# Kernel optimization log

Measured on AMD Instinct MI355X. Metric: run time of the kernel, lower is better.

The kernel has to match this reference:

```python
import jax, jax.numpy as jnp
import numpy as np

DIM = 128   # dim
KS = 3      # kernel_size
N = 8       # temporal frames (hard-coded n=8 in module)
B = 4       # clip batch -> 2D batch = B*N = 32
H = W = 64
EPS = 1e-5

def _bn(x, g, b, m, v):
    # inference BatchNorm2d over channel axis 1 (NCHW)
    s = g * jax.lax.rsqrt(v + EPS)
    return x * s[None, :, None, None] + (b - m * s)[None, :, None, None]

def _bn_vec(x, g, b, m, v):
    # BatchNorm over last axis of (B, C)
    s = g * jax.lax.rsqrt(v + EPS)
    return x * s + (b - m * s)

def setup_inputs():
    key = jax.random.key(0)
    ks = iter(jax.random.split(key, 48))
    nrm = lambda shape, sc=0.05: jax.random.normal(next(ks), shape, jnp.float32) * sc
    uni = lambda shape: jax.random.uniform(next(ks), shape, jnp.float32, minval=0.5, maxval=1.5)
    def bn_p(c):
        return uni((c,)), nrm((c,)), nrm((c,)), uni((c,))  # gamma, beta, running_mean, running_var
    d = {}
    d["x"] = jax.random.normal(next(ks), (B * N, DIM, H, W), jnp.float32)
    d["w_key"] = nrm((DIM, DIM // 4, KS, 1, 1))                      # conv3d (k,1,1), groups=4, no bias
    d["bnk_g"], d["bnk_b"], d["bnk_m"], d["bnk_v"] = bn_p(DIM)
    d["w_e1"] = nrm((DIM // 2, 2 * DIM))                             # 1x1 conv, no bias
    d["bne_g"], d["bne_b"], d["bne_m"], d["bne_v"] = bn_p(DIM // 2)
    d["w_e2"] = nrm((KS * DIM // 4, DIM // 2))
    d["b_e2"] = nrm((KS * DIM // 4,))
    d["gn_g"] = uni((KS * DIM // 4,))
    d["gn_b"] = nrm((KS * DIM // 4,))
    d["w_1x1"] = nrm((DIM, DIM))                                     # 1x1 conv, no bias
    d["bn1_g"], d["bn1_b"], d["bn1_m"], d["bn1_v"] = bn_p(DIM)
    d["bn2_g"], d["bn2_b"], d["bn2_m"], d["bn2_v"] = bn_p(DIM)
    d["w_se1"] = nrm((DIM, DIM))                                     # attn_chs = max(dim*2//2, 32) = dim
    d["b_se1"] = nrm((DIM,))
    d["bnse_g"], d["bnse_b"], d["bnse_m"], d["bnse_v"] = bn_p(DIM)
    d["w_se2"] = nrm((2 * DIM, DIM))
    d["b_se2"] = nrm((2 * DIM,))
    return d

def reference(x, w_key, bnk_g, bnk_b, bnk_m, bnk_v, w_e1, bne_g, bne_b, bne_m, bne_v,
              w_e2, b_e2, gn_g, gn_b, w_1x1, bn1_g, bn1_b, bn1_m, bn1_v,
              bn2_g, bn2_b, bn2_m, bn2_v, w_se1, b_se1, bnse_g, bnse_b, bnse_m, bnse_v,
              w_se2, b_se2):
    B2, C, Hh, Ww = x.shape
    b = B2 // N
    # --- key_embed: temporal grouped conv3d + BN + ReLU ---
    x5 = x.reshape(b, N, C, Hh, Ww).transpose(0, 2, 1, 3, 4)          # b c n h w
    kk = jax.lax.conv_general_dilated(
        x5, w_key, (1, 1, 1), ((KS // 2, KS // 2), (0, 0), (0, 0)),
        dimension_numbers=('NCDHW', 'OIDHW', 'NCDHW'), feature_group_count=4)
    k2d = kk.transpose(0, 2, 1, 3, 4).reshape(B2, C, Hh, Ww)
    k2d = jax.nn.relu(_bn(k2d, bnk_g, bnk_b, bnk_m, bnk_v))
    # --- dynamic per-pixel temporal kernels ---
    qk = jnp.concatenate([x, k2d], axis=1)                            # (b n) 2c h w
    e = jax.nn.relu(_bn(jnp.einsum('bchw,oc->bohw', qk, w_e1), bne_g, bne_b, bne_m, bne_v))
    wd = jnp.einsum('bchw,oc->bohw', e, w_e2) + b_e2[None, :, None, None]
    # GroupNorm: num_groups = C//4, group size = KS channels -> normalize over (KS, H, W)
    wg = wd.reshape(B2, C // 4, KS, Hh, Ww)
    mu = wg.mean(axis=(2, 3, 4), keepdims=True)
    var = wg.var(axis=(2, 3, 4), keepdims=True)
    wg = (wg - mu) * jax.lax.rsqrt(var + EPS)
    wd = wg.reshape(B2, KS * C // 4, Hh, Ww) * gn_g[None, :, None, None] + gn_b[None, :, None, None]
    wd = wd.reshape(B2, C // 4, KS, Hh, Ww)                           # w.view(b, c//4, 1, k, h, w) with c-dim squeezed
    # --- value path: 1x1 conv + BN, temporal unfold, dynamic aggregation ---
    v = _bn(jnp.einsum('bchw,oc->bohw', x, w_1x1), bn1_g, bn1_b, bn1_m, bn1_v)
    v5 = v.reshape(b, N, C, Hh, Ww).transpose(0, 2, 1, 3, 4)          # b c n h w
    pf = (KS - 1) // 2
    vp = jnp.pad(v5, ((0, 0), (0, 0), (pf, KS - 1 - pf), (0, 0), (0, 0)))
    unf = jnp.stack([vp[:, :, i:i + N] for i in range(KS)], axis=-1)  # b c n h w k (unfold dim=2)
    unf = unf.transpose(0, 2, 1, 3, 4, 5).reshape(B2, C // 4, 4, Hh, Ww, KS)  # (b n) c1 c2 h w k
    agg = jnp.einsum('nckhw,ncdhwk->ncdhw', wd, unf).reshape(B2, C, Hh, Ww)
    agg = _bn(agg, bn2_g, bn2_b, bn2_m, bn2_v)
    agg = agg * jax.nn.sigmoid(agg)                                   # SiLU
    # --- radix-2 split attention over (agg, k) ---
    x6 = agg.reshape(b, N, C, Hh, Ww).transpose(0, 2, 1, 3, 4)        # B C N H W
    k6 = k2d.reshape(b, N, C, Hh, Ww).transpose(0, 2, 1, 3, 4)
    u = jnp.stack([x6, k6], axis=2)                                   # B C 2 N H W
    gap = u.sum(axis=2).mean(axis=(2, 3, 4))                          # B C
    a = jax.nn.relu(_bn_vec(gap @ w_se1.T + b_se1, bnse_g, bnse_b, bnse_m, bnse_v))
    attn = jax.nn.softmax((a @ w_se2.T + b_se2).reshape(b, C, 2), axis=2)
    out = (u * attn[:, :, :, None, None, None]).sum(axis=2)           # B C N H W
    return out.transpose(0, 2, 1, 3, 4).reshape(B2, C, Hh, Ww)
```

## Files before the change

### kernel.cpp

```cpp
#include <hip/hip_runtime.h>

#define EPSV 1e-5f
typedef unsigned short u16;
typedef unsigned int u32;


typedef __attribute__((ext_vector_type(8))) __bf16 bf16x8;
typedef __attribute__((ext_vector_type(4))) float f32x4;
union ABcast { uint4 u; bf16x8 v; };

__device__ __forceinline__ u32 bfbits(float f) {
    u32 u = __float_as_uint(f);
    u += 0x7fff + ((u >> 16) & 1);
    return u >> 16;
}
__device__ __forceinline__ float bflo(u32 p) { return __uint_as_float(p << 16); }
__device__ __forceinline__ float bfhi(u32 p) { return __uint_as_float(p & 0xffff0000u); }

__global__ __launch_bounds__(256) void kW_pack(
    const float* __restrict__ wk, const float* __restrict__ w1,
    const float* __restrict__ we1, const float* __restrict__ we2,
    u32* __restrict__ wkF, u32* __restrict__ wB1,
    u32* __restrict__ wB, u32* __restrict__ wB2)
{
    int i = blockIdx.x * 256 + threadIdx.x;
    if (i < 6144) {
        int jj = i & 3;
        int ln = (i >> 2) & 63;
        int nt = (i >> 8) & 1;
        int rest = i >> 9;
        int grp = rest / 3, dk = rest % 3;
        int n = nt * 16 + (ln & 15);
        int k = (ln >> 4) * 8 + 2 * jj;
        int o = grp * 32 + n;
        wkF[i] = bfbits(wk[o * 96 + k * 3 + dk]) |
                 (bfbits(wk[o * 96 + (k + 1) * 3 + dk]) << 16);
    } else if (i < 14336) {
        int j2 = i - 6144;
        int jj = j2 & 3;
        int ln = (j2 >> 2) & 63;
        int nt = (j2 >> 8) & 7;
        int kb = j2 >> 11;
        int n = nt * 16 + (ln & 15);
        int k = kb * 32 + (ln >> 4) * 8 + 2 * jj;
        wB1[j2] = bfbits(w1[n * 128 + k]) | (bfbits(w1[n * 128 + k + 1]) << 16);
    } else if (i < 22528) {
        int j2 = i - 14336;
        int jj = j2 & 3;
        int ln = (j2 >> 2) & 63;
        int nt = (j2 >> 8) & 3;
        int kb = j2 >> 10;
        int n  = nt * 16 + (ln & 15);
        int k  = kb * 32 + (ln >> 4) * 8 + 2 * jj;
        wB[j2] = bfbits(we1[n * 256 + k]) | (bfbits(we1[n * 256 + k + 1]) << 16);
    } else if (i < 25600) {
        int j2 = i - 22528;
        int jj = j2 & 3;
        int ln = (j2 >> 2) & 63;
        int rest = j2 >> 8;
        int kb = rest / 6, nt = rest % 6;
        int n = nt * 16 + (ln & 15);
        int k = kb * 32 + (ln >> 4) * 8 + 2 * jj;
        wB2[j2] = bfbits(we2[n * 64 + k]) | (bfbits(we2[n * 64 + k + 1]) << 16);
    }
}

__global__ __launch_bounds__(256, 8) void kX_cvt(
    const float* __restrict__ x, u32* __restrict__ xh2)
{
    int qid = blockIdx.x * 256 + threadIdx.x;
    int px  = (qid & 1023) * 4;
    int c2g = qid >> 10;
    const float4 a = *(const float4*)(x + (c2g * 2) * 4096 + px);
    const float4 b = *(const float4*)(x + (c2g * 2 + 1) * 4096 + px);
    uint4 o;
    o.x = bfbits(a.x) | (bfbits(b.x) << 16);
    o.y = bfbits(a.y) | (bfbits(b.y) << 16);
    o.z = bfbits(a.z) | (bfbits(b.z) << 16);
    o.w = bfbits(a.w) | (bfbits(b.w) << 16);
    *(uint4*)(xh2 + c2g * 4096 + px) = o;
}

__global__ __launch_bounds__(256, 4) void kA_key(
    const u32* __restrict__ xh2, const u32* __restrict__ wkF,
    const float* __restrict__ g, const float* __restrict__ bb,
    const float* __restrict__ m, const float* __restrict__ vr,
    u32* __restrict__ k2dh2, float* __restrict__ gap)
{
    int tid  = threadIdx.x;
    int lane = tid & 63;
    int q    = __builtin_amdgcn_readfirstlane(tid >> 6);
    int blk  = blockIdx.x;
    int tile = blk & 15;
    int grp  = (blk >> 4) & 3;
    int b2   = blk >> 6;
    int px0  = tile * 256;
    int bi = b2 >> 3, ni = b2 & 7;
    int lrow = lane & 15, lk = lane >> 4;
    const uint4* wkF4 = (const uint4*)wkF;

    f32x4 acc[4][2];
    #pragma unroll
    for (int mt = 0; mt < 4; ++mt)
        #pragma unroll
        for (int nt = 0; nt < 2; ++nt)
            acc[mt][nt] = (f32x4){0.f, 0.f, 0.f, 0.f};

    int pxA[4];
    #pragma unroll
    for (int mt = 0; mt < 4; ++mt) pxA[mt] = px0 + (4 * q + mt) * 16 + lrow;

    #pragma unroll
    for (int dk = 0; dk < 3; ++dk) {
        int nf = ni + dk - 1;
        if (nf >= 0 && nf < 8) {
            const u32* src = xh2 + ((bi * 8 + nf) * 64 + grp * 16) * 4096;
            int c2b = (lk * 4) * 4096;
            ABcast a[4];
            #pragma unroll
            for (int mt = 0; mt < 4; ++mt) {
                a[mt].u.x = src[c2b         + pxA[mt]];
                a[mt].u.y = src[c2b + 4096  + pxA[mt]];
                a[mt].u.z = src[c2b + 8192  + pxA[mt]];
                a[mt].u.w = src[c2b + 12288 + pxA[mt]];
            }
            #pragma unroll
            for (int nt = 0; nt < 2; ++nt) {
                ABcast bfr;
                bfr.u = wkF4[((grp * 3 + dk) * 2 + nt) * 64 + lane];
                #pragma unroll
                for (int mt = 0; mt < 4; ++mt)
                    acc[mt][nt] = __builtin_amdgcn_mfma_f32_16x16x32_bf16(
                        a[mt].v, bfr.v, acc[mt][nt], 0, 0, 0);
            }
        }
    }

    __shared__ float ssum[32][4];
    #pragma unroll
    for (int nt = 0; nt < 2; ++nt) {
        int ch = grp * 32 + nt * 16 + lrow;
        float s = g[ch] * rsqrtf(vr[ch] + EPSV);
        float t = bb[ch] - m[ch] * s;
        float lsum = 0.f;
        #pragma unroll
        for (int mt = 0; mt < 4; ++mt) {
            float r0 = fmaxf(fmaf(acc[mt][nt].x, s, t), 0.f);
            float r1 = fmaxf(fmaf(acc[mt][nt].y, s, t), 0.f);
            float r2 = fmaxf(fmaf(acc[mt][nt].z, s, t), 0.f);
            float r3 = fmaxf(fmaf(acc[mt][nt].w, s, t), 0.f);
            lsum += r0 + r1 + r2 + r3;
            float p0 = __shfl_xor(r0, 1, 64);
            float p1 = __shfl_xor(r1, 1, 64);
            float p2 = __shfl_xor(r2, 1, 64);
            float p3 = __shfl_xor(r3, 1, 64);
            if (!(lane & 1)) {
                int c2out = grp * 16 + nt * 8 + (lrow >> 1);
                uint4 pk;
                pk.x = bfbits(r0) | (bfbits(p0) << 16);
                pk.y = bfbits(r1) | (bfbits(p1) << 16);
                pk.z = bfbits(r2) | (bfbits(p2) << 16);
                pk.w = bfbits(r3) | (bfbits(p3) << 16);
                *(uint4*)(k2dh2 + (b2 * 64 + c2out) * 4096 +
                          px0 + (4 * q + mt) * 16 + lk * 4) = pk;
            }
        }
        lsum += __shfl_xor(lsum, 16, 64);
        lsum += __shfl_xor(lsum, 32, 64);
        if (lane < 16) ssum[nt * 16 + lrow][q] = lsum;
    }
    __syncthreads();
    if (tid < 32) {
        float* sr = ssum[tid];
        atomicAdd(&gap[bi * 128 + grp * 32 + tid], sr[0] + sr[1] + sr[2] + sr[3]);
    }
}

__global__ __launch_bounds__(256, 3) void kB_val(
    const u32* __restrict__ xh2, const u32* __restrict__ wB1,
    const float* __restrict__ g, const float* __restrict__ bb,
    const float* __restrict__ m, const float* __restrict__ vr,
    u16* __restrict__ vh)
{
    int tid  = threadIdx.x;
    int lane = tid & 63;
    int q    = __builtin_amdgcn_readfirstlane(tid >> 6);
    int tile = blockIdx.x & 31;
    int b2   = blockIdx.x >> 5;
    int px0  = tile * 128;
    int lrow = lane & 15, lk = lane >> 4;

    const u32* xb = xh2 + b2 * 64 * 4096;
    const uint4* wB14 = (const uint4*)wB1;

    f32x4 acc[2][8];
    #pragma unroll
    for (int mt = 0; mt < 2; ++mt)
        #pragma unroll
        for (int nt = 0; nt < 8; ++nt)
            acc[mt][nt] = (f32x4){0.f, 0.f, 0.f, 0.f};

    int pxA0 = px0 + (2 * q) * 16 + lrow;
    int pxA1 = pxA0 + 16;

    #pragma unroll
    for (int kblk = 0; kblk < 4; ++kblk) {
        int c2b = (kblk * 16 + lk * 4) * 4096;
        ABcast a0, a1;
        a0.u.x = xb[c2b         + pxA0];
        a0.u.y = xb[c2b + 4096  + pxA0];
        a0.u.z = xb[c2b + 8192  + pxA0];
        a0.u.w = xb[c2b + 12288 + pxA0];
        a1.u.x = xb[c2b         + pxA1];
        a1.u.y = xb[c2b + 4096  + pxA1];
        a1.u.z = xb[c2b + 8192  + pxA1];
        a1.u.w = xb[c2b + 12288 + pxA1];
        #pragma unroll
        for (int nt = 0; nt < 8; ++nt) {
            ABcast bfr;
            bfr.u = wB14[(kblk * 8 + nt) * 64 + lane];
            acc[0][nt] = __builtin_amdgcn_mfma_f32_16x16x32_bf16(a0.v, bfr.v, acc[0][nt], 0, 0, 0);
            acc[1][nt] = __builtin_amdgcn_mfma_f32_16x16x32_bf16(a1.v, bfr.v, acc[1][nt], 0, 0, 0);
        }
    }

    #pragma unroll
    for (int nt = 0; nt < 8; ++nt) {
        int ch = nt * 16 + lrow;
        float s = g[ch] * rsqrtf(vr[ch] + EPSV);
        float t = bb[ch] - m[ch] * s;
        #pragma unroll
        for (int mt = 0; mt < 2; ++mt) {
            float r0 = fmaf(acc[mt][nt].x, s, t);
            float r1 = fmaf(acc[mt][nt].y, s, t);
            float r2 = fmaf(acc[mt][nt].z, s, t);
            float r3 = fmaf(acc[mt][nt].w, s, t);
            uint2 pk;
            pk.x = bfbits(r0) | (bfbits(r1) << 16);
            pk.y = bfbits(r2) | (bfbits(r3) << 16);
            *(uint2*)(vh + (b2 * 128 + ch) * 4096 +
                      px0 + (2 * q + mt) * 16 + lk * 4) = pk;
        }
    }
}

__global__ __launch_bounds__(256, 3) void kC_wd(
    const u32* __restrict__ xh2, const u32* __restrict__ k2dh2,
    const u32* __restrict__ wB,
    const float* __restrict__ eg, const float* __restrict__ eb,
    const float* __restrict__ em, const float* __restrict__ ev,
    const u32* __restrict__ wB2, const float* __restrict__ be2,
    u16* __restrict__ wdh, float* __restrict__ gnsum, float* __restrict__ gnsq)
{
    int tid  = threadIdx.x;
    int lane = tid & 63;
    int q    = __builtin_amdgcn_readfirstlane(tid >> 6);
    int tile = blockIdx.x & 31;
    int b2   = blockIdx.x >> 5;
    int px0  = tile * 128;
    int lrow = lane & 15;
    int lk   = lane >> 4;

    const u32* xb = xh2   + b2 * 64 * 4096;
    const u32* kb = k2dh2 + b2 * 64 * 4096;
    const uint4* wB4 = (const uint4*)wB;

    f32x4 acc[2][4];
    #pragma unroll
    for (int mt = 0; mt < 2; ++mt)
        #pragma unroll
        for (int nt = 0; nt < 4; ++nt)
            acc[mt][nt] = (f32x4){0.f, 0.f, 0.f, 0.f};

    int pxA0 = px0 + (2 * q) * 16 + lrow;
    int pxA1 = pxA0 + 16;

    #pragma unroll
    for (int kblk = 0; kblk < 8; ++kblk) {
        const u32* src = (kblk < 4) ? xb : kb;
        int c2b = (((kblk & 3) * 16) + lk * 4) * 4096;
        ABcast a0, a1;
        a0.u.x = src[c2b         + pxA0];
        a0.u.y = src[c2b + 4096  + pxA0];
        a0.u.z = src[c2b + 8192  + pxA0];
        a0.u.w = src[c2b + 12288 + pxA0];
        a1.u.x = src[c2b         + pxA1];
        a1.u.y = src[c2b + 4096  + pxA1];
        a1.u.z = src[c2b + 8192  + pxA1];
        a1.u.w = src[c2b + 12288 + pxA1];
        #pragma unroll
        for (int nt = 0; nt < 4; ++nt) {
            ABcast bfr;
            bfr.u = wB4[(kblk * 4 + nt) * 64 + lane];
            acc[0][nt] = __builtin_amdgcn_mfma_f32_16x16x32_bf16(a0.v, bfr.v, acc[0][nt], 0, 0, 0);
            acc[1][nt] = __builtin_amdgcn_mfma_f32_16x16x32_bf16(a1.v, bfr.v, acc[1][nt], 0, 0, 0);
        }
    }

    __shared__ __align__(16) u32 e_s2[32][132];
    #pragma unroll
    for (int nt = 0; nt < 4; ++nt) {
        int ch = nt * 16 + lrow;
        float s = eg[ch] * rsqrtf(ev[ch] + EPSV);
        float t = eb[ch] - em[ch] * s;
        #pragma unroll
        for (int mt = 0; mt < 2; ++mt) {
            float r0 = fmaxf(fmaf(acc[mt][nt].x, s, t), 0.f);
            float r1 = fmaxf(fmaf(acc[mt][nt].y, s, t), 0.f);
            float r2 = fmaxf(fmaf(acc[mt][nt].z, s, t), 0.f);
            float r3 = fmaxf(fmaf(acc[mt][nt].w, s, t), 0.f);
            float p0 = __shfl_xor(r0, 1, 64);
            float p1 = __shfl_xor(r1, 1, 64);
            float p2 = __shfl_xor(r2, 1, 64);
            float p3 = __shfl_xor(r3, 1, 64);
            if (!(lane & 1)) {
                uint4 pk;
                pk.x = bfbits(r0) | (bfbits(p0) << 16);
                pk.y = bfbits(r1) | (bfbits(p1) << 16);
                pk.z = bfbits(r2) | (bfbits(p2) << 16);
                pk.w = bfbits(r3) | (bfbits(p3) << 16);
                *(uint4*)&e_s2[nt * 8 + (lrow >> 1)][(2 * q + mt) * 16 + lk * 4] = pk;
            }
        }
    }
    __syncthreads();

    const uint4* wB24 = (const uint4*)wB2;
    f32x4 acc2[2][6];
    #pragma unroll
    for (int mt = 0; mt < 2; ++mt)
        #pragma unroll
        for (int nt = 0; nt < 6; ++nt)
            acc2[mt][nt] = (f32x4){0.f, 0.f, 0.f, 0.f};

    #pragma unroll
    for (int kb2 = 0; kb2 < 2; ++kb2) {
        int c2r = kb2 * 16 + lk * 4;
        ABcast a0, a1;
        int pl0 = (2 * q) * 16 + lrow;
        int pl1 = pl0 + 16;
        a0.u.x = e_s2[c2r + 0][pl0];
        a0.u.y = e_s2[c2r + 1][pl0];
        a0.u.z = e_s2[c2r + 2][pl0];
        a0.u.w = e_s2[c2r + 3][pl0];
        a1.u.x = e_s2[c2r + 0][pl1];
        a1.u.y = e_s2[c2r + 1][pl1];
        a1.u.z = e_s2[c2r + 2][pl1];
        a1.u.w = e_s2[c2r + 3][pl1];
        #pragma unroll
        for (int nt = 0; nt < 6; ++nt) {
            ABcast bfr;
            bfr.u = wB24[(kb2 * 6 + nt) * 64 + lane];
            acc2[0][nt] = __builtin_amdgcn_mfma_f32_16x16x32_bf16(a0.v, bfr.v, acc2[0][nt], 0, 0, 0);
            acc2[1][nt] = __builtin_amdgcn_mfma_f32_16x16x32_bf16(a1.v, bfr.v, acc2[1][nt], 0, 0, 0);
        }
    }

    __shared__ float s_sum[96][4], s_sq[96][4];
    #pragma unroll
    for (int nt = 0; nt < 6; ++nt) {
        int ch = nt * 16 + lrow;
        float bias = be2[ch];
        float lsum = 0.f, lsq = 0.f;
        #pragma unroll
        for (int mt = 0; mt < 2; ++mt) {
            float v0 = acc2[mt][nt].x + bias;
            float v1 = acc2[mt][nt].y + bias;
            float v2 = acc2[mt][nt].z + bias;
            float v3 = acc2[mt][nt].w + bias;
            uint2 pk;
            pk.x = bfbits(v0) | (bfbits(v1) << 16);
            pk.y = bfbits(v2) | (bfbits(v3) << 16);
            *(uint2*)(wdh + (b2 * 96 + ch) * 4096 +
                      px0 + (2 * q + mt) * 16 + lk * 4) = pk;
            lsum += v0 + v1 + v2 + v3;
            lsq  += v0 * v0 + v1 * v1 + v2 * v2 + v3 * v3;
        }
        lsum += __shfl_xor(lsum, 16, 64);
        lsum += __shfl_xor(lsum, 32, 64);
        lsq  += __shfl_xor(lsq, 16, 64);
        lsq  += __shfl_xor(lsq, 32, 64);
        if (lane < 16) { s_sum[ch][q] = lsum; s_sq[ch][q] = lsq; }
    }
    __syncthreads();
    if (tid < 32) {
        float ss = 0.f, sq = 0.f;
        #pragma unroll
        for (int j = 0; j < 3; ++j) {
            int ch = tid * 3 + j;
            ss += s_sum[ch][0] + s_sum[ch][1] + s_sum[ch][2] + s_sum[ch][3];
            sq += s_sq[ch][0] + s_sq[ch][1] + s_sq[ch][2] + s_sq[ch][3];
        }
        atomicAdd(&gnsum[b2 * 32 + tid], ss);
        atomicAdd(&gnsq [b2 * 32 + tid], sq);
    }
}

__global__ __launch_bounds__(256) void kC2_gn(
    const float* __restrict__ gnsum, const float* __restrict__ gnsq,
    float* __restrict__ gnmean, float* __restrict__ gnrstd)
{
    int idx = blockIdx.x * 256 + threadIdx.x;
    const float inv = 1.f / 12288.f;
    float mu  = gnsum[idx] * inv;
    float var = fmaf(gnsq[idx], inv, -mu * mu);
    gnmean[idx] = mu;
    gnrstd[idx] = rsqrtf(fmaxf(var, 0.f) + EPSV);
}

__global__ __launch_bounds__(256, 8) void kD_agg(
    const u16* __restrict__ wdh, const u16* __restrict__ vh,
    const float* __restrict__ gnmean, const float* __restrict__ gnrstd,
    const float* __restrict__ gng, const float* __restrict__ gnb,
    const float* __restrict__ g, const float* __restrict__ bb,
    const float* __restrict__ m, const float* __restrict__ vr,
    u16* __restrict__ aggh, float* __restrict__ gap)
{
    int blk   = blockIdx.x;
    int strip = blk & 7;
    int c1    = (blk >> 3) & 31;
    int bi    = blk >> 8;
    int px0   = strip * 512 + threadIdx.x * 2;

    float sch[4], tch[4], gl[4];
    #pragma unroll
    for (int ch = 0; ch < 4; ++ch) {
        int c = c1 * 4 + ch;
        float s = g[c] * rsqrtf(vr[c] + EPSV);
        sch[ch] = s; tch[ch] = bb[c] - m[c] * s; gl[ch] = 0.f;
    }
    float gg[3], gb[3];
    #pragma unroll
    for (int k = 0; k < 3; ++k) { gg[k] = gng[c1 * 3 + k]; gb[k] = gnb[c1 * 3 + k]; }

    float2 vreg[4][3];
    #pragma unroll
    for (int ch = 0; ch < 4; ++ch) {
        vreg[ch][0] = make_float2(0.f, 0.f);
        u32 v1u = *(const u32*)(vh + ((bi * 8 + 0) * 128 + c1 * 4 + ch) * 4096 + px0);
        u32 v2u = *(const u32*)(vh + ((bi * 8 + 1) * 128 + c1 * 4 + ch) * 4096 + px0);
        vreg[ch][1] = make_float2(bflo(v1u), bfhi(v1u));
        vreg[ch][2] = make_float2(bflo(v2u), bfhi(v2u));
    }

    for (int ni = 0; ni < 8; ++ni) {
        int b2 = bi * 8 + ni;
        float mu = gnmean[b2 * 32 + c1], rs = gnrstd[b2 * 32 + c1];
        float2 wn[3];
        #pragma unroll
        for (int k = 0; k < 3; ++k) {
            int nf = ni + k - 1;
            if (nf >= 0 && nf < 8) {
                u32 wvu = *(const u32*)(wdh + ((b2 * 96 + c1 * 3 + k) * 4096 + px0));
                wn[k].x = fmaf((bflo(wvu) - mu) * rs, gg[k], gb[k]);
                wn[k].y = fmaf((bfhi(wvu) - mu) * rs, gg[k], gb[k]);
            } else {
                wn[k] = make_float2(0.f, 0.f);
            }
        }
        #pragma unroll
        for (int ch = 0; ch < 4; ++ch) {
            float a0 = 0.f, a1 = 0.f;
            #pragma unroll
            for (int k = 0; k < 3; ++k) {
                a0 = fmaf(wn[k].x, vreg[ch][k].x, a0);
                a1 = fmaf(wn[k].y, vreg[ch][k].y, a1);
            }
            float y0 = fmaf(a0, sch[ch], tch[ch]);
            float y1 = fmaf(a1, sch[ch], tch[ch]);
            float r0 = y0 / (1.f + __expf(-y0));
            float r1 = y1 / (1.f + __expf(-y1));
            *(u32*)(aggh + (b2 * 128 + c1 * 4 + ch) * 4096 + px0) =
                bfbits(r0) | (bfbits(r1) << 16);
            gl[ch] += r0 + r1;
        }
        if (ni < 7) {
            #pragma unroll
            for (int ch = 0; ch < 4; ++ch) {
                vreg[ch][0] = vreg[ch][1];
                vreg[ch][1] = vreg[ch][2];
                if (ni + 2 < 8) {
                    u32 vu = *(const u32*)(vh + ((bi * 8 + ni + 2) * 128 + c1 * 4 + ch) * 4096 + px0);
                    vreg[ch][2] = make_float2(bflo(vu), bfhi(vu));
                }
            }
        }
    }

    __shared__ float sm[4][4];
    int lane = threadIdx.x & 63, wid = threadIdx.x >> 6;
    #pragma unroll
    for (int ch = 0; ch < 4; ++ch) {
        float s = gl[ch];
        #pragma unroll
        for (int off = 32; off; off >>= 1) s += __shfl_down(s, off, 64);
        if (lane == 0) sm[ch][wid] = s;
    }
    __syncthreads();
    if (threadIdx.x < 4) {
        float* sr = sm[threadIdx.x];
        atomicAdd(&gap[bi * 128 + c1 * 4 + threadIdx.x], sr[0] + sr[1] + sr[2] + sr[3]);
    }
}

__global__ __launch_bounds__(256) void kE1_a(
    const float* __restrict__ gap,
    const float* __restrict__ w1, const float* __restrict__ b1,
    const float* __restrict__ g, const float* __restrict__ bb,
    const float* __restrict__ m, const float* __restrict__ vr,
    float* __restrict__ a_buf)
{
    int idx = blockIdx.x * 256 + threadIdx.x;
    int bi = idx >> 7, oc = idx & 127;
    float acc = b1[oc];
    const float* gp = gap + bi * 128;
    const float* wp = w1 + oc * 128;
    for (int c = 0; c < 128; c += 4) {
        const float4 w4 = *(const float4*)(wp + c);
        acc = fmaf(gp[c + 0] * (1.f / 32768.f), w4.x, acc);
        acc = fmaf(gp[c + 1] * (1.f / 32768.f), w4.y, acc);
        acc = fmaf(gp[c + 2] * (1.f / 32768.f), w4.z, acc);
        acc = fmaf(gp[c + 3] * (1.f / 32768.f), w4.w, acc);
    }
    float s = g[oc] * rsqrtf(vr[oc] + EPSV);
    a_buf[bi * 128 + oc] = fmaxf(fmaf(acc, s, bb[oc] - m[oc] * s), 0.f);
}

__global__ __launch_bounds__(256) void kE2_attn(
    const float* __restrict__ a_buf,
    const float* __restrict__ w2, const float* __restrict__ b2v,
    float* __restrict__ attn)
{
    int idx = blockIdx.x * 256 + threadIdx.x;
    int bi = idx >> 7, cc = idx & 127;
    float l0 = b2v[cc * 2], l1 = b2v[cc * 2 + 1];
    const float* ap  = a_buf + bi * 128;
    const float* w0p = w2 + (cc * 2) * 128;
    const float* w1p = w2 + (cc * 2 + 1) * 128;
    for (int j = 0; j < 128; j += 4) {
        const float4 wa4 = *(const float4*)(w0p + j);
        const float4 wb4 = *(const float4*)(w1p + j);
        l0 = fmaf(ap[j + 0], wa4.x, l0); l1 = fmaf(ap[j + 0], wb4.x, l1);
        l0 = fmaf(ap[j + 1], wa4.y, l0); l1 = fmaf(ap[j + 1], wb4.y, l1);
        l0 = fmaf(ap[j + 2], wa4.z, l0); l1 = fmaf(ap[j + 2], wb4.z, l1);
        l0 = fmaf(ap[j + 3], wa4.w, l0); l1 = fmaf(ap[j + 3], wb4.w, l1);
    }
    float mx = fmaxf(l0, l1);
    float e0 = __expf(l0 - mx), e1 = __expf(l1 - mx);
    float inv = 1.f / (e0 + e1);
    attn[bi * 256 + cc * 2]     = e0 * inv;
    attn[bi * 256 + cc * 2 + 1] = e1 * inv;
}

__global__ __launch_bounds__(256, 8) void kF_out(
    float* __restrict__ out, const u16* __restrict__ aggh,
    const u32* __restrict__ k2dh2, const float* __restrict__ attn)
{
    int blk   = blockIdx.x;
    int strip = blk & 3;
    int c2    = (blk >> 2) & 63;
    int b2    = blk >> 8;
    int bi    = b2 >> 3;
    int px0   = strip * 1024 + threadIdx.x * 4;

    float a0e = attn[bi * 256 + 4 * c2];
    float a1e = attn[bi * 256 + 4 * c2 + 1];
    float a0o = attn[bi * 256 + 4 * c2 + 2];
    float a1o = attn[bi * 256 + 4 * c2 + 3];

    uint4 kk = *(const uint4*)(k2dh2 + (b2 * 64 + c2) * 4096 + px0);
    uint2 g0 = *(const uint2*)(aggh + (b2 * 128 + 2 * c2) * 4096 + px0);
    uint2 g1 = *(const uint2*)(aggh + (b2 * 128 + 2 * c2 + 1) * 4096 + px0);

    float4 re, ro;
    re.x = fmaf(a0e, bflo(g0.x), a1e * bflo(kk.x));
    re.y = fmaf(a0e, bfhi(g0.x), a1e * bflo(kk.y));
    re.z = fmaf(a0e, bflo(g0.y), a1e * bflo(kk.z));
    re.w = fmaf(a0e, bfhi(g0.y), a1e * bflo(kk.w));
    ro.x = fmaf(a0o, bflo(g1.x), a1o * bfhi(kk.x));
    ro.y = fmaf(a0o, bfhi(g1.x), a1o * bfhi(kk.y));
    ro.z = fmaf(a0o, bflo(g1.y), a1o * bfhi(kk.z));
    ro.w = fmaf(a0o, bfhi(g1.y), a1o * bfhi(kk.w));
    *(float4*)(out + (b2 * 128 + 2 * c2) * 4096 + px0) = re;
    *(float4*)(out + (b2 * 128 + 2 * c2 + 1) * 4096 + px0) = ro;
}

extern "C" void kernel_launch(void* const* d_in, const int* in_sizes, int n_in,
                              void* d_out, int out_size, void* d_ws, size_t ws_size,
                              hipStream_t stream)
{
    const float* x      = (const float*)d_in[0];
    const float* w_key  = (const float*)d_in[1];
    const float* bnk_g  = (const float*)d_in[2];
    const float* bnk_b  = (const float*)d_in[3];
    const float* bnk_m  = (const float*)d_in[4];
    const float* bnk_v  = (const float*)d_in[5];
    const float* w_e1   = (const float*)d_in[6];
    const float* bne_g  = (const float*)d_in[7];
    const float* bne_b  = (const float*)d_in[8];
    const float* bne_m  = (const float*)d_in[9];
    const float* bne_v  = (const float*)d_in[10];
    const float* w_e2   = (const float*)d_in[11];
    const float* b_e2   = (const float*)d_in[12];
    const float* gn_g   = (const float*)d_in[13];
    const float* gn_b   = (const float*)d_in[14];
    const float* w_1x1  = (const float*)d_in[15];
    const float* bn1_g  = (const float*)d_in[16];
    const float* bn1_b  = (const float*)d_in[17];
    const float* bn1_m  = (const float*)d_in[18];
    const float* bn1_v  = (const float*)d_in[19];
    const float* bn2_g  = (const float*)d_in[20];
    const float* bn2_b  = (const float*)d_in[21];
    const float* bn2_m  = (const float*)d_in[22];
    const float* bn2_v  = (const float*)d_in[23];
    const float* w_se1  = (const float*)d_in[24];
    const float* b_se1  = (const float*)d_in[25];
    const float* bnse_g = (const float*)d_in[26];
    const float* bnse_b = (const float*)d_in[27];
    const float* bnse_m = (const float*)d_in[28];
    const float* bnse_v = (const float*)d_in[29];
    const float* w_se2  = (const float*)d_in[30];
    const float* b_se2  = (const float*)d_in[31];

    float* ws    = (float*)d_ws;
    u32*  xh2   = (u32*)ws;
    u32*  k2dh2 = (u32*)(ws + 8388608);
    u16*  vh    = (u16*)(ws + 16777216);
    u16*  aggh  = (u16*)(ws + 25165824);
    u16*  wdh   = (u16*)(ws + 33554432);
    u32*  wkF   = (u32*)(ws + 39845888);
    u32*  wB1   = wkF + 6144;
    u32*  wB    = wB1 + 8192;
    u32*  wB2   = wB + 8192;
    float* st   = ws + 46137344;
    float* gnsum  = st;
    float* gnsq   = st + 1024;
    float* gap    = st + 2048;
    float* gnmean = st + 2560;
    float* gnrstd = st + 3584;
    float* attn   = st + 4608;
    float* a_buf  = st;

    hipMemsetAsync(gnsum, 0, 2560 * sizeof(float), stream);

    kW_pack<<<100, 256, 0, stream>>>(w_key, w_1x1, w_e1, w_e2, wkF, wB1, wB, wB2);
    kX_cvt<<<8192, 256, 0, stream>>>(x, xh2);
    kA_key<<<2048, 256, 0, stream>>>(xh2, wkF, bnk_g, bnk_b, bnk_m, bnk_v, k2dh2, gap);
    kB_val<<<1024, 256, 0, stream>>>(xh2, wB1, bn1_g, bn1_b, bn1_m, bn1_v, vh);
    kC_wd<<<1024, 256, 0, stream>>>(xh2, k2dh2, wB, bne_g, bne_b, bne_m, bne_v,
                                    wB2, b_e2, wdh, gnsum, gnsq);
    kC2_gn<<<4, 256, 0, stream>>>(gnsum, gnsq, gnmean, gnrstd);
    kD_agg<<<1024, 256, 0, stream>>>(wdh, vh, gnmean, gnrstd, gn_g, gn_b,
                                     bn2_g, bn2_b, bn2_m, bn2_v, aggh, gap);
    kE1_a<<<2, 256, 0, stream>>>(gap, w_se1, b_se1, bnse_g, bnse_b, bnse_m, bnse_v, a_buf);
    kE2_attn<<<2, 256, 0, stream>>>(a_buf, w_se2, b_se2, attn);
    kF_out<<<8192, 256, 0, stream>>>((float*)d_out, aggh, k2dh2, attn);
}
```

Baseline: 169.4 us.

## Store bf16 input in 8-channel interleaved layout for 16-byte MFMA operand loads

```diff
diff --git a/kernel.cpp b/kernel.cpp
--- a/kernel.cpp
+++ b/kernel.cpp
@@ -66,23 +66,22 @@
 }
 
 __global__ __launch_bounds__(256, 8) void kX_cvt(
-    const float* __restrict__ x, u32* __restrict__ xh2)
+    const float* __restrict__ x, u32* __restrict__ xq)
 {
     int qid = blockIdx.x * 256 + threadIdx.x;
-    int px  = (qid & 1023) * 4;
-    int c2g = qid >> 10;
-    const float4 a = *(const float4*)(x + (c2g * 2) * 4096 + px);
-    const float4 b = *(const float4*)(x + (c2g * 2 + 1) * 4096 + px);
+    int px  = qid & 4095;
+    int c8g = qid >> 12;
+    const float* xp = x + (c8g * 8) * 4096 + px;
     uint4 o;
-    o.x = bfbits(a.x) | (bfbits(b.x) << 16);
-    o.y = bfbits(a.y) | (bfbits(b.y) << 16);
-    o.z = bfbits(a.z) | (bfbits(b.z) << 16);
-    o.w = bfbits(a.w) | (bfbits(b.w) << 16);
-    *(uint4*)(xh2 + c2g * 4096 + px) = o;
+    o.x = bfbits(xp[0])        | (bfbits(xp[4096])     << 16);
+    o.y = bfbits(xp[2 * 4096]) | (bfbits(xp[3 * 4096]) << 16);
+    o.z = bfbits(xp[4 * 4096]) | (bfbits(xp[5 * 4096]) << 16);
+    o.w = bfbits(xp[6 * 4096]) | (bfbits(xp[7 * 4096]) << 16);
+    *(uint4*)(xq + (c8g * 4096 + px) * 4) = o;
 }
 
 __global__ __launch_bounds__(256, 4) void kA_key(
-    const u32* __restrict__ xh2, const u32* __restrict__ wkF,
+    const u32* __restrict__ xq, const u32* __restrict__ wkF,
     const float* __restrict__ g, const float* __restrict__ bb,
     const float* __restrict__ m, const float* __restrict__ vr,
     u32* __restrict__ k2dh2, float* __restrict__ gap)
@@ -114,16 +113,11 @@
     for (int dk = 0; dk < 3; ++dk) {
         int nf = ni + dk - 1;
         if (nf >= 0 && nf < 8) {
-            const u32* src = xh2 + ((bi * 8 + nf) * 64 + grp * 16) * 4096;
-            int c2b = (lk * 4) * 4096;
+            const u32* src = xq + (((bi * 8 + nf) * 16 + grp * 4 + lk) * 4096) * 4;
             ABcast a[4];
             #pragma unroll
-            for (int mt = 0; mt < 4; ++mt) {
-                a[mt].u.x = src[c2b         + pxA[mt]];
-                a[mt].u.y = src[c2b + 4096  + pxA[mt]];
-                a[mt].u.z = src[c2b + 8192  + pxA[mt]];
-                a[mt].u.w = src[c2b + 12288 + pxA[mt]];
-            }
+            for (int mt = 0; mt < 4; ++mt)
+                a[mt].u = *(const uint4*)(src + pxA[mt] * 4);
             #pragma unroll
             for (int nt = 0; nt < 2; ++nt) {
                 ABcast bfr;
@@ -177,7 +171,7 @@
 }
 
 __global__ __launch_bounds__(256, 3) void kB_val(
-    const u32* __restrict__ xh2, const u32* __restrict__ wB1,
+    const u32* __restrict__ xq, const u32* __restrict__ wB1,
     const float* __restrict__ g, const float* __restrict__ bb,
     const float* __restrict__ m, const float* __restrict__ vr,
     u16* __restrict__ vh)
@@ -190,7 +184,6 @@
     int px0  = tile * 128;
     int lrow = lane & 15, lk = lane >> 4;
 
-    const u32* xb = xh2 + b2 * 64 * 4096;
     const uint4* wB14 = (const uint4*)wB1;
 
     f32x4 acc[2][8];
@@ -205,16 +198,10 @@
 
     #pragma unroll
     for (int kblk = 0; kblk < 4; ++kblk) {
-        int c2b = (kblk * 16 + lk * 4) * 4096;
+        const u32* src = xq + ((b2 * 16 + kblk * 4 + lk) * 4096) * 4;
         ABcast a0, a1;
-        a0.u.x = xb[c2b         + pxA0];
-        a0.u.y = xb[c2b + 4096  + pxA0];
-        a0.u.z = xb[c2b + 8192  + pxA0];
-        a0.u.w = xb[c2b + 12288 + pxA0];
-        a1.u.x = xb[c2b         + pxA1];
-        a1.u.y = xb[c2b + 4096  + pxA1];
-        a1.u.z = xb[c2b + 8192  + pxA1];
-        a1.u.w = xb[c2b + 12288 + pxA1];
+        a0.u = *(const uint4*)(src + pxA0 * 4);
+        a1.u = *(const uint4*)(src + pxA1 * 4);
         #pragma unroll
         for (int nt = 0; nt < 8; ++nt) {
             ABcast bfr;
@@ -245,7 +232,7 @@
 }
 
 __global__ __launch_bounds__(256, 3) void kC_wd(
-    const u32* __restrict__ xh2, const u32* __restrict__ k2dh2,
+    const u32* __restrict__ xq, const u32* __restrict__ k2dh2,
     const u32* __restrict__ wB,
     const float* __restrict__ eg, const float* __restrict__ eb,
     const float* __restrict__ em, const float* __restrict__ ev,
@@ -261,7 +248,6 @@
     int lrow = lane & 15;
     int lk   = lane >> 4;
 
-    const u32* xb = xh2   + b2 * 64 * 4096;
     const u32* kb = k2dh2 + b2 * 64 * 4096;
     const uint4* wB4 = (const uint4*)wB;
 
@@ -276,18 +262,31 @@
     int pxA1 = pxA0 + 16;
 
     #pragma unroll
-    for (int kblk = 0; kblk < 8; ++kblk) {
-        const u32* src = (kblk < 4) ? xb : kb;
+    for (int kblk = 0; kblk < 4; ++kblk) {
+        const u32* src = xq + ((b2 * 16 + kblk * 4 + lk) * 4096) * 4;
+        ABcast a0, a1;
+        a0.u = *(const uint4*)(src + pxA0 * 4);
+        a1.u = *(const uint4*)(src + pxA1 * 4);
+        #pragma unroll
+        for (int nt = 0; nt < 4; ++nt) {
+            ABcast bfr;
+            bfr.u = wB4[(kblk * 4 + nt) * 64 + lane];
+            acc[0][nt] = __builtin_amdgcn_mfma_f32_16x16x32_bf16(a0.v, bfr.v, acc[0][nt], 0, 0, 0);
+            acc[1][nt] = __builtin_amdgcn_mfma_f32_16x16x32_bf16(a1.v, bfr.v, acc[1][nt], 0, 0, 0);
+        }
+    }
+    #pragma unroll
+    for (int kblk = 4; kblk < 8; ++kblk) {
         int c2b = (((kblk & 3) * 16) + lk * 4) * 4096;
         ABcast a0, a1;
-        a0.u.x = src[c2b         + pxA0];
-        a0.u.y = src[c2b + 4096  + pxA0];
-        a0.u.z = src[c2b + 8192  + pxA0];
-        a0.u.w = src[c2b + 12288 + pxA0];
-        a1.u.x = src[c2b         + pxA1];
-        a1.u.y = src[c2b + 4096  + pxA1];
-        a1.u.z = src[c2b + 8192  + pxA1];
-        a1.u.w = src[c2b + 12288 + pxA1];
+        a0.u.x = kb[c2b         + pxA0];
+        a0.u.y = kb[c2b + 4096  + pxA0];
+        a0.u.z = kb[c2b + 8192  + pxA0];
+        a0.u.w = kb[c2b + 12288 + pxA0];
+        a1.u.x = kb[c2b         + pxA1];
+        a1.u.y = kb[c2b + 4096  + pxA1];
+        a1.u.z = kb[c2b + 8192  + pxA1];
+        a1.u.w = kb[c2b + 12288 + pxA1];
         #pragma unroll
         for (int nt = 0; nt < 4; ++nt) {
             ABcast bfr;
@@ -623,7 +622,7 @@
     const float* b_se2  = (const float*)d_in[31];
 
     float* ws    = (float*)d_ws;
-    u32*  xh2   = (u32*)ws;
+    u32*  xq    = (u32*)ws;
     u32*  k2dh2 = (u32*)(ws + 8388608);
     u16*  vh    = (u16*)(ws + 16777216);
     u16*  aggh  = (u16*)(ws + 25165824);
@@ -644,10 +643,10 @@
     hipMemsetAsync(gnsum, 0, 2560 * sizeof(float), stream);
 
     kW_pack<<<100, 256, 0, stream>>>(w_key, w_1x1, w_e1, w_e2, wkF, wB1, wB, wB2);
-    kX_cvt<<<8192, 256, 0, stream>>>(x, xh2);
-    kA_key<<<2048, 256, 0, stream>>>(xh2, wkF, bnk_g, bnk_b, bnk_m, bnk_v, k2dh2, gap);
-    kB_val<<<1024, 256, 0, stream>>>(xh2, wB1, bn1_g, bn1_b, bn1_m, bn1_v, vh);
-    kC_wd<<<1024, 256, 0, stream>>>(xh2, k2dh2, wB, bne_g, bne_b, bne_m, bne_v,
+    kX_cvt<<<8192, 256, 0, stream>>>(x, xq);
+    kA_key<<<2048, 256, 0, stream>>>(xq, wkF, bnk_g, bnk_b, bnk_m, bnk_v, k2dh2, gap);
+    kB_val<<<1024, 256, 0, stream>>>(xq, wB1, bn1_g, bn1_b, bn1_m, bn1_v, vh);
+    kC_wd<<<1024, 256, 0, stream>>>(xq, k2dh2, wB, bne_g, bne_b, bne_m, bne_v,
                                     wB2, b_e2, wdh, gnsum, gnsq);
     kC2_gn<<<4, 256, 0, stream>>>(gnsum, gnsq, gnmean, gnrstd);
     kD_agg<<<1024, 256, 0, stream>>>(wdh, vh, gnmean, gnrstd, gn_g, gn_b,
```

New measurement: 152.2 us. 10.1% less time.
